# Performance work log

Measured on AMD Instinct MI355X. Metric: run time of the kernel, lower is better.

The kernel has to match this reference:

```python
import jax, jax.numpy as jnp
import numpy as np

N = 100000
E = 3200000
NFEAT = 256
NHID = 128
NCLASS = 64


def setup_inputs() -> dict:
    key = jax.random.key(0)
    ks = jax.random.split(key, 10)
    x = jax.random.normal(ks[0], (N, NFEAT), dtype=jnp.float32)
    src = jax.random.randint(ks[1], (E,), 0, N, dtype=jnp.int32).astype(jnp.int64)
    dst = jax.random.randint(ks[2], (E,), 0, N, dtype=jnp.int32).astype(jnp.int64)
    # Glorot-ish init for GraphConv weights
    def w(k, i, o):
        return jax.random.normal(k, (i, o), dtype=jnp.float32) * (1.0 / np.sqrt(i))
    W0 = w(ks[3], NFEAT, NHID)
    b0 = jnp.zeros((NHID,), dtype=jnp.float32)
    W1 = w(ks[4], NHID, NHID)
    b1 = jnp.zeros((NHID,), dtype=jnp.float32)
    W2 = w(ks[5], NHID, NCLASS)
    b2 = jnp.zeros((NCLASS,), dtype=jnp.float32)
    return {"x": x, "src": src, "dst": dst,
            "W0": W0, "b0": b0, "W1": W1, "b1": b1, "W2": W2, "b2": b2}


def _degree_norms(src, dst, dtype):
    ones = jnp.ones(src.shape, dtype)
    deg_out = jax.ops.segment_sum(ones, src, num_segments=N)
    deg_in = jax.ops.segment_sum(ones, dst, num_segments=N)
    # clamp zero degrees to avoid inf (DGL clamps to 1)
    n_src = jnp.where(deg_out > 0, deg_out, 1.0) ** -0.5
    n_dst = jnp.where(deg_in > 0, deg_in, 1.0) ** -0.5
    return n_src, n_dst


def _graph_conv(h, src, dst, n_src, n_dst, W, b):
    # weight first (math-equivalent to DGL ordering), then normalized SpMM
    h = h @ W                              # [N, out]
    msg = h[src] * n_src[src][:, None]     # [E, out] gather + src norm
    agg = jax.ops.segment_sum(msg, dst, num_segments=N)  # [N, out]
    return agg * n_dst[:, None] + b


def reference(x, src, dst, W0, b0, W1, b1, W2, b2):
    n_src, n_dst = _degree_norms(src, dst, x.dtype)
    h = _graph_conv(x, src, dst, n_src, n_dst, W0, b0)
    # dropout is identity in eval mode
    h = _graph_conv(h, src, dst, n_src, n_dst, W1, b1)
    h = _graph_conv(h, src, dst, n_src, n_dst, W2, b2)
    return jax.nn.softmax(h, axis=1)
```

## Files before the change

### kernel.cpp

```cpp
#include <hip/hip_runtime.h>
#include <hip/hip_bf16.h>

#define N_NODES 100000
#define N_EDGES 3200000
#define NFEAT 256
#define NHID 128
#define NCLASS 64
#define SCAN_B 1024
#define NB_SCAN ((N_NODES + SCAN_B - 1) / SCAN_B)
#define NVEC4 (N_EDGES / 4)
#define RANGE (N_NODES / 8)
#define NSL 64

typedef unsigned int uint32;
typedef unsigned short ushort16;
typedef __attribute__((ext_vector_type(8))) short bf16x8;
typedef __attribute__((ext_vector_type(4))) float f32x4;

static __device__ __forceinline__ float b2f(ushort16 u) {
    union { float f; uint32 i; } c; c.i = ((uint32)u) << 16; return c.f;
}
static __device__ __forceinline__ ushort16 f2b(float f) {
    union { float f; uint32 i; } c; c.f = f;
    uint32 r = (c.i + 0x7FFFu + ((c.i >> 16) & 1u)) >> 16;
    return (ushort16)r;
}
static __device__ __forceinline__ float blo(uint32 u) {
    union { float f; uint32 i; } c; c.i = u << 16; return c.f;
}
static __device__ __forceinline__ float bhi(uint32 u) {
    union { float f; uint32 i; } c; c.i = u & 0xFFFF0000u; return c.f;
}

__global__ __launch_bounds__(256) void k_hist(const int4* __restrict__ src4,
                                              const int4* __restrict__ dst4,
                                              uint32* __restrict__ scratch) {
    __shared__ uint32 h[RANGE];
    int g = blockIdx.x & 7, sl = blockIdx.x >> 3;
    int lo = g * RANGE, hi = lo + RANGE;
    for (int i = threadIdx.x; i < RANGE; i += 256) h[i] = 0u;
    __syncthreads();
    for (int t = sl * 256 + threadIdx.x; t < NVEC4; t += NSL * 256) {
        int4 s = src4[t], d = dst4[t];
        if (s.x >= lo && s.x < hi) atomicAdd(&h[s.x - lo], 1u);
        if (s.y >= lo && s.y < hi) atomicAdd(&h[s.y - lo], 1u);
        if (s.z >= lo && s.z < hi) atomicAdd(&h[s.z - lo], 1u);
        if (s.w >= lo && s.w < hi) atomicAdd(&h[s.w - lo], 1u);
        if (d.x >= lo && d.x < hi) atomicAdd(&h[d.x - lo], 65536u);
        if (d.y >= lo && d.y < hi) atomicAdd(&h[d.y - lo], 65536u);
        if (d.z >= lo && d.z < hi) atomicAdd(&h[d.z - lo], 65536u);
        if (d.w >= lo && d.w < hi) atomicAdd(&h[d.w - lo], 65536u);
    }
    __syncthreads();
    uint32* dstp = scratch + ((size_t)(g * NSL + sl)) * RANGE;
    for (int i = threadIdx.x; i < RANGE; i += 256) dstp[i] = h[i];
}

__global__ void k_sumdeg(const uint32* __restrict__ scratch, int* __restrict__ deg_in,
                         float* __restrict__ n_src, float* __restrict__ n_dst) {
    int i = blockIdx.x * blockDim.x + threadIdx.x;
    if (i >= N_NODES) return;
    int g = i / RANGE, r = i - g * RANGE;
    const uint32* base = scratch + (size_t)g * NSL * RANGE + r;
    uint32 so = 0, di = 0;
    for (int s = 0; s < NSL; s++) {
        uint32 v = base[(size_t)s * RANGE];
        so += v & 0xFFFFu;
        di += v >> 16;
    }
    deg_in[i] = (int)di;
    uint32 so1 = so < 1u ? 1u : so;
    uint32 di1 = di < 1u ? 1u : di;
    n_src[i] = rsqrtf((float)so1);
    n_dst[i] = rsqrtf((float)di1);
}

__global__ void k_scan1(const int* __restrict__ deg_in, int* __restrict__ row_ptr,
                        int* __restrict__ blk_sums) {
    __shared__ int sh[SCAN_B];
    int i = blockIdx.x * SCAN_B + threadIdx.x;
    int v = (i < N_NODES) ? deg_in[i] : 0;
    sh[threadIdx.x] = v;
    __syncthreads();
    for (int o = 1; o < SCAN_B; o <<= 1) {
        int t = 0;
        if ((int)threadIdx.x >= o) t = sh[threadIdx.x - o];
        __syncthreads();
        sh[threadIdx.x] += t;
        __syncthreads();
    }
    if (i < N_NODES) row_ptr[i] = sh[threadIdx.x] - v;
    if (threadIdx.x == SCAN_B - 1) blk_sums[blockIdx.x] = sh[SCAN_B - 1];
}

__global__ void k_scan2(int* __restrict__ blk_sums) {
    if (threadIdx.x == 0 && blockIdx.x == 0) {
        int acc = 0;
        for (int b = 0; b < NB_SCAN; b++) { int v = blk_sums[b]; blk_sums[b] = acc; acc += v; }
        blk_sums[NB_SCAN] = acc;
    }
}

__global__ void k_scan3(const int* __restrict__ blk_sums, int* __restrict__ row_ptr) {
    int i = blockIdx.x * SCAN_B + threadIdx.x;
    if (i < N_NODES) row_ptr[i] += blk_sums[blockIdx.x];
    if (i == 0) row_ptr[N_NODES] = blk_sums[NB_SCAN];
}

__global__ void k_offsets(uint32* __restrict__ scratch, const int* __restrict__ row_ptr) {
    int i = blockIdx.x * blockDim.x + threadIdx.x;
    if (i >= N_NODES) return;
    int g = i / RANGE, r = i - g * RANGE;
    uint32* base = scratch + (size_t)g * NSL * RANGE + r;
    uint32 run = (uint32)row_ptr[i];
    for (int s = 0; s < NSL; s++) {
        uint32 v = base[(size_t)s * RANGE];
        base[(size_t)s * RANGE] = run;
        run += v >> 16;
    }
}

__global__ __launch_bounds__(256) void k_fill2(const int4* __restrict__ src4,
                                               const int4* __restrict__ dst4,
                                               const uint32* __restrict__ scratch,
                                               int* __restrict__ col) {
    __shared__ uint32 cur[RANGE];
    int g = blockIdx.x & 7, sl = blockIdx.x >> 3;
    int lo = g * RANGE, hi = lo + RANGE;
    const uint32* base = scratch + ((size_t)(g * NSL + sl)) * RANGE;
    for (int i = threadIdx.x; i < RANGE; i += 256) cur[i] = base[i];
    __syncthreads();
    for (int t = sl * 256 + threadIdx.x; t < NVEC4; t += NSL * 256) {
        int4 s = src4[t], d = dst4[t];
        if (d.x >= lo && d.x < hi) { uint32 p = atomicAdd(&cur[d.x - lo], 1u); col[p] = s.x; }
        if (d.y >= lo && d.y < hi) { uint32 p = atomicAdd(&cur[d.y - lo], 1u); col[p] = s.y; }
        if (d.z >= lo && d.z < hi) { uint32 p = atomicAdd(&cur[d.z - lo], 1u); col[p] = s.z; }
        if (d.w >= lo && d.w < hi) { uint32 p = atomicAdd(&cur[d.w - lo], 1u); col[p] = s.w; }
    }
}

__global__ void k_w01(const float* __restrict__ W0, const float* __restrict__ W1,
                      float* __restrict__ W01) {
    __shared__ float row[NHID];
    int r = blockIdx.x, c = threadIdx.x;
    row[c] = W0[r * NHID + c];
    __syncthreads();
    float acc = 0.f;
    for (int k = 0; k < NHID; k++) acc += row[k] * W1[k * NHID + c];
    W01[r * NHID + c] = acc;
}

__global__ void k_wc(const float* __restrict__ W01, const float* __restrict__ W2,
                     float* __restrict__ Wc, ushort16* __restrict__ Wt) {
    __shared__ float row[NHID];
    int r = blockIdx.x, c = threadIdx.x;
    row[c] = W01[r * NHID + c];
    row[c + 64] = W01[r * NHID + c + 64];
    __syncthreads();
    float acc = 0.f;
    for (int k = 0; k < NHID; k++) acc += row[k] * W2[k * NCLASS + c];
    Wc[r * NCLASS + c] = acc;
    Wt[(size_t)c * NFEAT + r] = f2b(acc);
}

__global__ void k_bv(const float* __restrict__ b0, const float* __restrict__ W1,
                     const float* __restrict__ b1, const float* __restrict__ W2,
                     float* __restrict__ bv) {
    __shared__ float tmp[NHID];
    int c = threadIdx.x;
    for (int cc = c; cc < NHID; cc += 64) {
        float a = 0.f;
        for (int k = 0; k < NHID; k++) a += b0[k] * W1[k * NHID + cc];
        tmp[cc] = a;
    }
    __syncthreads();
    float a1 = 0.f, a2 = 0.f;
    for (int k = 0; k < NHID; k++) {
        float wv = W2[k * NCLASS + c];
        a1 += tmp[k] * wv;
        a2 += b1[k] * wv;
    }
    bv[c] = a1;
    bv[64 + c] = a2;
}

__global__ __launch_bounds__(256) void k_gemm_y(const float* __restrict__ x,
                                                const ushort16* __restrict__ Wt,
                                                ushort16* __restrict__ y) {
    int tid = threadIdx.x;
    int wid = tid >> 6, lane = tid & 63;
    int q = lane >> 4, r = lane & 15;
    int rowbase = blockIdx.x * 64 + wid * 16;
    int rowld = min(rowbase + r, N_NODES - 1);
    const float* xp = x + (size_t)rowld * NFEAT + q * 8;

    float4 alo[8], ahi[8];
#pragma unroll
    for (int kt = 0; kt < 8; kt++) {
        alo[kt] = *(const float4*)(xp + kt * 32);
        ahi[kt] = *(const float4*)(xp + kt * 32 + 4);
    }

    f32x4 acc0 = {0.f, 0.f, 0.f, 0.f};
    f32x4 acc1 = {0.f, 0.f, 0.f, 0.f};
    f32x4 acc2 = {0.f, 0.f, 0.f, 0.f};
    f32x4 acc3 = {0.f, 0.f, 0.f, 0.f};

#pragma unroll
    for (int kt = 0; kt < 8; kt++) {
        bf16x8 af;
        af[0] = (short)f2b(alo[kt].x); af[1] = (short)f2b(alo[kt].y);
        af[2] = (short)f2b(alo[kt].z); af[3] = (short)f2b(alo[kt].w);
        af[4] = (short)f2b(ahi[kt].x); af[5] = (short)f2b(ahi[kt].y);
        af[6] = (short)f2b(ahi[kt].z); af[7] = (short)f2b(ahi[kt].w);
        const int ko = kt * 32 + q * 8;
        bf16x8 b0 = *(const bf16x8*)(Wt + (size_t)(0 * 16 + r) * NFEAT + ko);
        bf16x8 b1 = *(const bf16x8*)(Wt + (size_t)(1 * 16 + r) * NFEAT + ko);
        bf16x8 b2 = *(const bf16x8*)(Wt + (size_t)(2 * 16 + r) * NFEAT + ko);
        bf16x8 b3 = *(const bf16x8*)(Wt + (size_t)(3 * 16 + r) * NFEAT + ko);
        acc0 = __builtin_amdgcn_mfma_f32_16x16x32_bf16(af, b0, acc0, 0, 0, 0);
        acc1 = __builtin_amdgcn_mfma_f32_16x16x32_bf16(af, b1, acc1, 0, 0, 0);
        acc2 = __builtin_amdgcn_mfma_f32_16x16x32_bf16(af, b2, acc2, 0, 0, 0);
        acc3 = __builtin_amdgcn_mfma_f32_16x16x32_bf16(af, b3, acc3, 0, 0, 0);
    }

    int srow0 = rowbase + q * 4;
#pragma unroll
    for (int i = 0; i < 4; i++) {
        int rr = srow0 + i;
        if (rr < N_NODES) {
            ushort16* yp = y + (size_t)rr * NCLASS + r;
            yp[0]  = f2b(acc0[i]);
            yp[16] = f2b(acc1[i]);
            yp[32] = f2b(acc2[i]);
            yp[48] = f2b(acc3[i]);
        }
    }
}

template <int PASS>
__global__ __launch_bounds__(256) void k_agg(
        const int* __restrict__ row_ptr, const int* __restrict__ col,
        const float* __restrict__ n_src, const float* __restrict__ n_dst,
        const ushort16* __restrict__ in, ushort16* __restrict__ out,
        float* __restrict__ outf,
        const float* __restrict__ tin, float* __restrict__ tout,
        const float* __restrict__ t1, const float* __restrict__ t2,
        const float* __restrict__ bv, const float* __restrict__ b2) {
    int wid = threadIdx.x >> 6, lane = threadIdx.x & 63;
    int node = blockIdx.x * 4 + wid;
    if (node >= N_NODES) return;
    int g = lane >> 3, sub = lane & 7;
    int s = row_ptr[node], e = row_ptr[node + 1];
    const uint4* inr = (const uint4*)in;

    float acc0 = 0.f, acc1 = 0.f, acc2 = 0.f, acc3 = 0.f;
    float acc4 = 0.f, acc5 = 0.f, acc6 = 0.f, acc7 = 0.f;
    float accs = 0.f;

#define CH(P)                                                                  \
    {                                                                          \
        int p_ = (P);                                                          \
        bool v_ = p_ < e;                                                      \
        int j_ = v_ ? col[p_] : 0;                                             \
        float ns_ = n_src[j_];                                                 \
        if (!v_) ns_ = 0.f;                                                    \
        uint4 u_ = inr[(size_t)j_ * 8 + sub];                                  \
        acc0 += ns_ * blo(u_.x); acc1 += ns_ * bhi(u_.x);                      \
        acc2 += ns_ * blo(u_.y); acc3 += ns_ * bhi(u_.y);                      \
        acc4 += ns_ * blo(u_.z); acc5 += ns_ * bhi(u_.z);                      \
        acc6 += ns_ * blo(u_.w); acc7 += ns_ * bhi(u_.w);                      \
        if (PASS == 1) accs += ns_;                                            \
        if (PASS == 2) accs += ns_ * tin[j_];                                  \
    }

    for (int base = s; base < e; base += 32) {
        CH(base + g)
        CH(base + 8 + g)
        CH(base + 16 + g)
        CH(base + 24 + g)
    }
#undef CH

#pragma unroll
    for (int off = 8; off <= 32; off <<= 1) {
        acc0 += __shfl_xor(acc0, off, 64);
        acc1 += __shfl_xor(acc1, off, 64);
        acc2 += __shfl_xor(acc2, off, 64);
        acc3 += __shfl_xor(acc3, off, 64);
        acc4 += __shfl_xor(acc4, off, 64);
        acc5 += __shfl_xor(acc5, off, 64);
        acc6 += __shfl_xor(acc6, off, 64);
        acc7 += __shfl_xor(acc7, off, 64);
        if (PASS != 3) accs += __shfl_xor(accs, off, 64);
    }

    float nd = n_dst[node];
    if (PASS == 3) {
        float t2n = t2[node], t1n = t1[node];
        const float* bvA = bv + sub * 8;
        const float* bvB = bv + 64 + sub * 8;
        const float* b2p = b2 + sub * 8;
        float v0 = acc0 * nd + t2n * bvA[0] + t1n * bvB[0] + b2p[0];
        float v1 = acc1 * nd + t2n * bvA[1] + t1n * bvB[1] + b2p[1];
        float v2 = acc2 * nd + t2n * bvA[2] + t1n * bvB[2] + b2p[2];
        float v3 = acc3 * nd + t2n * bvA[3] + t1n * bvB[3] + b2p[3];
        float v4 = acc4 * nd + t2n * bvA[4] + t1n * bvB[4] + b2p[4];
        float v5 = acc5 * nd + t2n * bvA[5] + t1n * bvB[5] + b2p[5];
        float v6 = acc6 * nd + t2n * bvA[6] + t1n * bvB[6] + b2p[6];
        float v7 = acc7 * nd + t2n * bvA[7] + t1n * bvB[7] + b2p[7];
        float m = fmaxf(fmaxf(fmaxf(v0, v1), fmaxf(v2, v3)),
                        fmaxf(fmaxf(v4, v5), fmaxf(v6, v7)));
#pragma unroll
        for (int off = 1; off <= 4; off <<= 1) m = fmaxf(m, __shfl_xor(m, off, 64));
        float e0 = __expf(v0 - m), e1 = __expf(v1 - m), e2 = __expf(v2 - m), e3 = __expf(v3 - m);
        float e4 = __expf(v4 - m), e5 = __expf(v5 - m), e6 = __expf(v6 - m), e7 = __expf(v7 - m);
        float sum = ((e0 + e1) + (e2 + e3)) + ((e4 + e5) + (e6 + e7));
#pragma unroll
        for (int off = 1; off <= 4; off <<= 1) sum += __shfl_xor(sum, off, 64);
        float r = 1.0f / sum;
        if (g == 0) {
            float4 o0 = {e0 * r, e1 * r, e2 * r, e3 * r};
            float4 o1 = {e4 * r, e5 * r, e6 * r, e7 * r};
            float4* op = (float4*)(outf + (size_t)node * NCLASS + sub * 8);
            op[0] = o0;
            op[1] = o1;
        }
    } else {
        if (g == 0) {
            uint32 w0 = (uint32)f2b(acc0 * nd) | ((uint32)f2b(acc1 * nd) << 16);
            uint32 w1 = (uint32)f2b(acc2 * nd) | ((uint32)f2b(acc3 * nd) << 16);
            uint32 w2 = (uint32)f2b(acc4 * nd) | ((uint32)f2b(acc5 * nd) << 16);
            uint32 w3 = (uint32)f2b(acc6 * nd) | ((uint32)f2b(acc7 * nd) << 16);
            uint4 w = {w0, w1, w2, w3};
            *((uint4*)(out + (size_t)node * NCLASS) + sub) = w;
        }
        if (lane == 0) tout[node] = accs * nd;
    }
}

extern "C" void kernel_launch(void* const* d_in, const int* in_sizes, int n_in,
                              void* d_out, int out_size, void* d_ws, size_t ws_size,
                              hipStream_t stream) {
    const float* x   = (const float*)d_in[0];
    const int*   src = (const int*)d_in[1];
    const int*   dst = (const int*)d_in[2];
    const float* W0  = (const float*)d_in[3];
    const float* b0  = (const float*)d_in[4];
    const float* W1  = (const float*)d_in[5];
    const float* b1  = (const float*)d_in[6];
    const float* W2  = (const float*)d_in[7];
    const float* b2  = (const float*)d_in[8];
    float* out = (float*)d_out;

    size_t off = 0;
    auto alloc = [&](size_t bytes) {
        void* p = (char*)d_ws + off;
        off = (off + bytes + 255) & ~(size_t)255;
        return p;
    };
    int*      deg_in   = (int*)alloc(N_NODES * 4);
    float*    n_src    = (float*)alloc(N_NODES * 4);
    float*    n_dst    = (float*)alloc(N_NODES * 4);
    int*      row_ptr  = (int*)alloc((N_NODES + 1) * 4);
    int*      blk_sums = (int*)alloc((NB_SCAN + 1) * 4);
    int*      col      = (int*)alloc((size_t)N_EDGES * 4);
    uint32*   scratch  = (uint32*)alloc((size_t)8 * NSL * RANGE * 4);
    float*    W01      = (float*)alloc(NFEAT * NHID * 4);
    float*    Wc       = (float*)alloc(NFEAT * NCLASS * 4);
    ushort16* Wt       = (ushort16*)alloc((size_t)NFEAT * NCLASS * 2);
    float*    bv       = (float*)alloc(128 * 4);
    float*    t1       = (float*)alloc(N_NODES * 4);
    float*    t2       = (float*)alloc(N_NODES * 4);
    ushort16* bufB1    = (ushort16*)alloc((size_t)N_NODES * NCLASS * 2);
    ushort16* bufB2    = (ushort16*)alloc((size_t)N_NODES * NCLASS * 2);
    (void)ws_size; (void)in_sizes; (void)n_in; (void)out_size;

    const int TB = 256;
    const int NBn = (N_NODES + TB - 1) / TB;
    const int NW = (N_NODES + 3) / 4;
    const int GP = 8 * NSL;

    k_hist<<<GP, TB, 0, stream>>>((const int4*)src, (const int4*)dst, scratch);
    k_sumdeg<<<NBn, TB, 0, stream>>>(scratch, deg_in, n_src, n_dst);
    k_scan1<<<NB_SCAN, SCAN_B, 0, stream>>>(deg_in, row_ptr, blk_sums);
    k_scan2<<<1, 64, 0, stream>>>(blk_sums);
    k_scan3<<<NB_SCAN, SCAN_B, 0, stream>>>(blk_sums, row_ptr);
    k_offsets<<<NBn, TB, 0, stream>>>(scratch, row_ptr);
    k_fill2<<<GP, TB, 0, stream>>>((const int4*)src, (const int4*)dst, scratch, col);

    k_w01<<<NFEAT, NHID, 0, stream>>>(W0, W1, W01);
    k_wc<<<NFEAT, NCLASS, 0, stream>>>(W01, W2, Wc, Wt);
    k_bv<<<1, NCLASS, 0, stream>>>(b0, W1, b1, W2, bv);

    k_gemm_y<<<(N_NODES + 63) / 64, 256, 0, stream>>>(x, Wt, bufB1);

    k_agg<1><<<NW, 256, 0, stream>>>(row_ptr, col, n_src, n_dst, bufB1, bufB2, nullptr,
                                     nullptr, t1, nullptr, nullptr, nullptr, nullptr);
    k_agg<2><<<NW, 256, 0, stream>>>(row_ptr, col, n_src, n_dst, bufB2, bufB1, nullptr,
                                     t1, t2, nullptr, nullptr, nullptr, nullptr);
    k_agg<3><<<NW, 256, 0, stream>>>(row_ptr, col, n_src, n_dst, bufB1, nullptr, out,
                                     nullptr, nullptr, t1, t2, bv, b2);
}
```

Baseline: 539.0 us.

## Pre-scale features by source norm and use zero sentinel row in aggregation

Folds the n_src scaling into the producer (GEMM epilogue and each aggregation's output), so the per-edge gather no longer loads n_src[j] or multiplies by it. Adds a zeroed sentinel node N_NODES so padded edges index a zero row instead of being masked, and uses 32-bit byte offsets for addressing. The per-node scalar sums are also precomputed with the source norm folded in. This removes one dependent random load and several FMAs per edge, at the cost of an extra sentinel wave and slightly different bf16 rounding.

```diff
diff --git a/kernel.cpp b/kernel.cpp
--- a/kernel.cpp
+++ b/kernel.cpp
@@ -16,6 +16,7 @@
 typedef unsigned short ushort16;
 typedef __attribute__((ext_vector_type(8))) short bf16x8;
 typedef __attribute__((ext_vector_type(4))) float f32x4;
+typedef __attribute__((ext_vector_type(2))) float f32x2;
 
 static __device__ __forceinline__ float b2f(ushort16 u) {
     union { float f; uint32 i; } c; c.i = ((uint32)u) << 16; return c.f;
@@ -30,6 +31,9 @@
 }
 static __device__ __forceinline__ float bhi(uint32 u) {
     union { float f; uint32 i; } c; c.i = u & 0xFFFF0000u; return c.f;
+}
+static __device__ __forceinline__ uint32 pack2(float a, float b) {
+    return (uint32)f2b(a) | ((uint32)f2b(b) << 16);
 }
 
 __global__ __launch_bounds__(256) void k_hist(const int4* __restrict__ src4,
@@ -60,6 +64,7 @@
                          float* __restrict__ n_src, float* __restrict__ n_dst) {
     int i = blockIdx.x * blockDim.x + threadIdx.x;
     if (i >= N_NODES) return;
+    if (i == 0) n_src[N_NODES] = 0.f;
     int g = i / RANGE, r = i - g * RANGE;
     const uint32* base = scratch + (size_t)g * NSL * RANGE + r;
     uint32 so = 0, di = 0;
@@ -186,6 +191,7 @@
 
 __global__ __launch_bounds__(256) void k_gemm_y(const float* __restrict__ x,
                                                 const ushort16* __restrict__ Wt,
+                                                const float* __restrict__ n_src,
                                                 ushort16* __restrict__ y) {
     int tid = threadIdx.x;
     int wid = tid >> 6, lane = tid & 63;
@@ -229,11 +235,15 @@
     for (int i = 0; i < 4; i++) {
         int rr = srow0 + i;
         if (rr < N_NODES) {
+            float ns = n_src[rr];
             ushort16* yp = y + (size_t)rr * NCLASS + r;
-            yp[0]  = f2b(acc0[i]);
-            yp[16] = f2b(acc1[i]);
-            yp[32] = f2b(acc2[i]);
-            yp[48] = f2b(acc3[i]);
+            yp[0]  = f2b(acc0[i] * ns);
+            yp[16] = f2b(acc1[i] * ns);
+            yp[32] = f2b(acc2[i] * ns);
+            yp[48] = f2b(acc3[i] * ns);
+        } else if (rr == N_NODES) {
+            ushort16* yp = y + (size_t)rr * NCLASS + r;
+            yp[0] = 0; yp[16] = 0; yp[32] = 0; yp[48] = 0;
         }
     }
 }
@@ -241,37 +251,53 @@
 template <int PASS>
 __global__ __launch_bounds__(256) void k_agg(
         const int* __restrict__ row_ptr, const int* __restrict__ col,
+        const float* __restrict__ wsrc,
         const float* __restrict__ n_src, const float* __restrict__ n_dst,
         const ushort16* __restrict__ in, ushort16* __restrict__ out,
         float* __restrict__ outf,
-        const float* __restrict__ tin, float* __restrict__ tout,
+        float* __restrict__ tsave, float* __restrict__ tssave,
         const float* __restrict__ t1, const float* __restrict__ t2,
         const float* __restrict__ bv, const float* __restrict__ b2) {
     int wid = threadIdx.x >> 6, lane = threadIdx.x & 63;
     int node = blockIdx.x * 4 + wid;
-    if (node >= N_NODES) return;
+    if (node > N_NODES) return;
     int g = lane >> 3, sub = lane & 7;
+
+    if (node == N_NODES) {
+        if (PASS != 3) {
+            if (g == 0) {
+                uint4 z = {0u, 0u, 0u, 0u};
+                *((uint4*)((char*)out + ((size_t)N_NODES << 7)) + sub) = z;
+            }
+            if (lane == 0) {
+                tsave[N_NODES] = 0.f;
+                if (PASS == 1) tssave[N_NODES] = 0.f;
+            }
+        }
+        return;
+    }
+
     int s = row_ptr[node], e = row_ptr[node + 1];
-    const uint4* inr = (const uint4*)in;
-
-    float acc0 = 0.f, acc1 = 0.f, acc2 = 0.f, acc3 = 0.f;
-    float acc4 = 0.f, acc5 = 0.f, acc6 = 0.f, acc7 = 0.f;
+    const char* inb = (const char*)in;
+    const char* wb  = (const char*)wsrc;
+    uint32 subo = (uint32)sub << 4;
+
+    f32x2 a0 = {0.f, 0.f}, a1 = {0.f, 0.f}, a2 = {0.f, 0.f}, a3 = {0.f, 0.f};
     float accs = 0.f;
 
 #define CH(P)                                                                  \
     {                                                                          \
         int p_ = (P);                                                          \
         bool v_ = p_ < e;                                                      \
-        int j_ = v_ ? col[p_] : 0;                                             \
-        float ns_ = n_src[j_];                                                 \
-        if (!v_) ns_ = 0.f;                                                    \
-        uint4 u_ = inr[(size_t)j_ * 8 + sub];                                  \
-        acc0 += ns_ * blo(u_.x); acc1 += ns_ * bhi(u_.x);                      \
-        acc2 += ns_ * blo(u_.y); acc3 += ns_ * bhi(u_.y);                      \
-        acc4 += ns_ * blo(u_.z); acc5 += ns_ * bhi(u_.z);                      \
-        acc6 += ns_ * blo(u_.w); acc7 += ns_ * bhi(u_.w);                      \
-        if (PASS == 1) accs += ns_;                                            \
-        if (PASS == 2) accs += ns_ * tin[j_];                                  \
+        int j_ = v_ ? col[p_] : N_NODES;                                       \
+        uint32 fo_ = ((uint32)j_ << 7) + subo;                                 \
+        uint4 u_ = *(const uint4*)(inb + fo_);                                 \
+        if (PASS != 3) accs += *(const float*)(wb + ((uint32)j_ << 2));        \
+        f32x2 q0; q0.x = blo(u_.x); q0.y = bhi(u_.x);                          \
+        f32x2 q1; q1.x = blo(u_.y); q1.y = bhi(u_.y);                          \
+        f32x2 q2; q2.x = blo(u_.z); q2.y = bhi(u_.z);                          \
+        f32x2 q3; q3.x = blo(u_.w); q3.y = bhi(u_.w);                          \
+        a0 += q0; a1 += q1; a2 += q2; a3 += q3;                                \
     }
 
     for (int base = s; base < e; base += 32) {
@@ -284,14 +310,10 @@
 
 #pragma unroll
     for (int off = 8; off <= 32; off <<= 1) {
-        acc0 += __shfl_xor(acc0, off, 64);
-        acc1 += __shfl_xor(acc1, off, 64);
-        acc2 += __shfl_xor(acc2, off, 64);
-        acc3 += __shfl_xor(acc3, off, 64);
-        acc4 += __shfl_xor(acc4, off, 64);
-        acc5 += __shfl_xor(acc5, off, 64);
-        acc6 += __shfl_xor(acc6, off, 64);
-        acc7 += __shfl_xor(acc7, off, 64);
+        a0.x += __shfl_xor(a0.x, off, 64); a0.y += __shfl_xor(a0.y, off, 64);
+        a1.x += __shfl_xor(a1.x, off, 64); a1.y += __shfl_xor(a1.y, off, 64);
+        a2.x += __shfl_xor(a2.x, off, 64); a2.y += __shfl_xor(a2.y, off, 64);
+        a3.x += __shfl_xor(a3.x, off, 64); a3.y += __shfl_xor(a3.y, off, 64);
         if (PASS != 3) accs += __shfl_xor(accs, off, 64);
     }
 
@@ -301,14 +323,14 @@
         const float* bvA = bv + sub * 8;
         const float* bvB = bv + 64 + sub * 8;
         const float* b2p = b2 + sub * 8;
-        float v0 = acc0 * nd + t2n * bvA[0] + t1n * bvB[0] + b2p[0];
-        float v1 = acc1 * nd + t2n * bvA[1] + t1n * bvB[1] + b2p[1];
-        float v2 = acc2 * nd + t2n * bvA[2] + t1n * bvB[2] + b2p[2];
-        float v3 = acc3 * nd + t2n * bvA[3] + t1n * bvB[3] + b2p[3];
-        float v4 = acc4 * nd + t2n * bvA[4] + t1n * bvB[4] + b2p[4];
-        float v5 = acc5 * nd + t2n * bvA[5] + t1n * bvB[5] + b2p[5];
-        float v6 = acc6 * nd + t2n * bvA[6] + t1n * bvB[6] + b2p[6];
-        float v7 = acc7 * nd + t2n * bvA[7] + t1n * bvB[7] + b2p[7];
+        float v0 = a0.x * nd + t2n * bvA[0] + t1n * bvB[0] + b2p[0];
+        float v1 = a0.y * nd + t2n * bvA[1] + t1n * bvB[1] + b2p[1];
+        float v2 = a1.x * nd + t2n * bvA[2] + t1n * bvB[2] + b2p[2];
+        float v3 = a1.y * nd + t2n * bvA[3] + t1n * bvB[3] + b2p[3];
+        float v4 = a2.x * nd + t2n * bvA[4] + t1n * bvB[4] + b2p[4];
+        float v5 = a2.y * nd + t2n * bvA[5] + t1n * bvB[5] + b2p[5];
+        float v6 = a3.x * nd + t2n * bvA[6] + t1n * bvB[6] + b2p[6];
+        float v7 = a3.y * nd + t2n * bvA[7] + t1n * bvB[7] + b2p[7];
         float m = fmaxf(fmaxf(fmaxf(v0, v1), fmaxf(v2, v3)),
                         fmaxf(fmaxf(v4, v5), fmaxf(v6, v7)));
 #pragma unroll
@@ -328,14 +350,19 @@
         }
     } else {
         if (g == 0) {
-            uint32 w0 = (uint32)f2b(acc0 * nd) | ((uint32)f2b(acc1 * nd) << 16);
-            uint32 w1 = (uint32)f2b(acc2 * nd) | ((uint32)f2b(acc3 * nd) << 16);
-            uint32 w2 = (uint32)f2b(acc4 * nd) | ((uint32)f2b(acc5 * nd) << 16);
-            uint32 w3 = (uint32)f2b(acc6 * nd) | ((uint32)f2b(acc7 * nd) << 16);
+            float sc = nd * n_src[node];
+            uint32 w0 = pack2(a0.x * sc, a0.y * sc);
+            uint32 w1 = pack2(a1.x * sc, a1.y * sc);
+            uint32 w2 = pack2(a2.x * sc, a2.y * sc);
+            uint32 w3 = pack2(a3.x * sc, a3.y * sc);
             uint4 w = {w0, w1, w2, w3};
-            *((uint4*)(out + (size_t)node * NCLASS) + sub) = w;
+            *((uint4*)((char*)out + ((size_t)node << 7)) + sub) = w;
         }
-        if (lane == 0) tout[node] = accs * nd;
+        if (lane == 0) {
+            float T = accs * nd;
+            tsave[node] = T;
+            if (PASS == 1) tssave[node] = T * n_src[node];
+        }
     }
 }
 
@@ -360,7 +387,7 @@
         return p;
     };
     int*      deg_in   = (int*)alloc(N_NODES * 4);
-    float*    n_src    = (float*)alloc(N_NODES * 4);
+    float*    n_src    = (float*)alloc((N_NODES + 1) * 4);
     float*    n_dst    = (float*)alloc(N_NODES * 4);
     int*      row_ptr  = (int*)alloc((N_NODES + 1) * 4);
     int*      blk_sums = (int*)alloc((NB_SCAN + 1) * 4);
@@ -370,15 +397,16 @@
     float*    Wc       = (float*)alloc(NFEAT * NCLASS * 4);
     ushort16* Wt       = (ushort16*)alloc((size_t)NFEAT * NCLASS * 2);
     float*    bv       = (float*)alloc(128 * 4);
-    float*    t1       = (float*)alloc(N_NODES * 4);
-    float*    t2       = (float*)alloc(N_NODES * 4);
-    ushort16* bufB1    = (ushort16*)alloc((size_t)N_NODES * NCLASS * 2);
-    ushort16* bufB2    = (ushort16*)alloc((size_t)N_NODES * NCLASS * 2);
+    float*    t1       = (float*)alloc((N_NODES + 1) * 4);
+    float*    t1s      = (float*)alloc((N_NODES + 1) * 4);
+    float*    t2       = (float*)alloc((N_NODES + 1) * 4);
+    ushort16* bufB1    = (ushort16*)alloc((size_t)(N_NODES + 1) * NCLASS * 2);
+    ushort16* bufB2    = (ushort16*)alloc((size_t)(N_NODES + 1) * NCLASS * 2);
     (void)ws_size; (void)in_sizes; (void)n_in; (void)out_size;
 
     const int TB = 256;
     const int NBn = (N_NODES + TB - 1) / TB;
-    const int NW = (N_NODES + 3) / 4;
+    const int NW = (N_NODES + 3) / 4 + 1;
     const int GP = 8 * NSL;
 
     k_hist<<<GP, TB, 0, stream>>>((const int4*)src, (const int4*)dst, scratch);
@@ -393,12 +421,12 @@
     k_wc<<<NFEAT, NCLASS, 0, stream>>>(W01, W2, Wc, Wt);
     k_bv<<<1, NCLASS, 0, stream>>>(b0, W1, b1, W2, bv);
 
-    k_gemm_y<<<(N_NODES + 63) / 64, 256, 0, stream>>>(x, Wt, bufB1);
-
-    k_agg<1><<<NW, 256, 0, stream>>>(row_ptr, col, n_src, n_dst, bufB1, bufB2, nullptr,
-                                     nullptr, t1, nullptr, nullptr, nullptr, nullptr);
-    k_agg<2><<<NW, 256, 0, stream>>>(row_ptr, col, n_src, n_dst, bufB2, bufB1, nullptr,
-                                     t1, t2, nullptr, nullptr, nullptr, nullptr);
-    k_agg<3><<<NW, 256, 0, stream>>>(row_ptr, col, n_src, n_dst, bufB1, nullptr, out,
-                                     nullptr, nullptr, t1, t2, bv, b2);
-}
+    k_gemm_y<<<(N_NODES + 64) / 64, 256, 0, stream>>>(x, Wt, n_src, bufB1);
+
+    k_agg<1><<<NW, 256, 0, stream>>>(row_ptr, col, n_src, n_src, n_dst, bufB1, bufB2,
+                                     nullptr, t1, t1s, nullptr, nullptr, nullptr, nullptr);
+    k_agg<2><<<NW, 256, 0, stream>>>(row_ptr, col, t1s, n_src, n_dst, bufB2, bufB1,
+                                     nullptr, t2, nullptr, nullptr, nullptr, nullptr, nullptr);
+    k_agg<3><<<NW, 256, 0, stream>>>(row_ptr, col, nullptr, n_src, n_dst, bufB1, nullptr,
+                                     out, nullptr, nullptr, t1, t2, bv, b2);
+}
```

Result: no change. 535.6 us (-0.6%).
